# Kernel tuning notes

Measured on AMD Instinct MI355X. Metric: run time of the kernel, lower is better.

## Reference

```python
import jax, jax.numpy as jnp
import numpy as np

# Static graph-batch geometry (equal-size graphs -> uniform per-graph k, jit-friendly)
B = 512        # number of graphs
N_PER = 2048   # nodes per graph
C = 64         # in_channels
DEG = 16       # average degree
K = 1024       # ceil(ratio * N_PER) with ratio = 0.5
N = B * N_PER
E = B * N_PER * DEG


def setup_inputs() -> dict:
    key = jax.random.key(0)
    k1, k2, k3 = jax.random.split(key, 3)
    x = jax.random.normal(k1, (N, C), dtype=jnp.float32)
    # edges are intra-graph: local endpoints in [0, N_PER) plus per-graph node offset
    local = jax.random.randint(k2, (2, E), 0, N_PER, dtype=jnp.int32)
    offs = jnp.repeat(jnp.arange(B, dtype=jnp.int32) * N_PER, N_PER * DEG)
    edge_index = local + offs[None, :]
    batch = jnp.repeat(jnp.arange(B, dtype=jnp.int32), N_PER)
    p = jax.random.normal(k3, (C,), dtype=jnp.float32)  # SelectTopK projection weight
    return {"x": x, "edge_index": edge_index, "batch": batch, "p": p}


def reference(x, edge_index, batch, p):
    # SelectTopK: y = tanh(x @ p / ||p||), per-graph top-k
    y = jnp.tanh(x @ p / jnp.linalg.norm(p))            # [N]
    scores, local_idx = jax.lax.top_k(y.reshape(B, N_PER), K)   # [B, K] each
    perm = (local_idx.astype(jnp.int32)
            + jnp.arange(B, dtype=jnp.int32)[:, None] * N_PER).reshape(-1)  # [B*K] global ids
    score = scores.reshape(-1)                          # [B*K]
    # gather + scale (multiplier == 1)
    x_out = x[perm] * score[:, None]                    # [B*K, C]
    # FilterEdges / connect: remap kept nodes to new contiguous ids, mask dropped edges
    node_map = jnp.full((N,), -1, dtype=jnp.int32).at[perm].set(
        jnp.arange(B * K, dtype=jnp.int32))
    new_src = node_map[edge_index[0]]
    new_dst = node_map[edge_index[1]]
    edge_mask = (new_src >= 0) & (new_dst >= 0)         # [E] which edges survive
    new_edge_index = jnp.where(edge_mask[None, :],
                               jnp.stack([new_src, new_dst]), -1)  # dropped edges = -1
    new_batch = batch[perm]
    return x_out, new_edge_index, new_batch, perm, score
```

## Files before the change

### kernel.cpp

```cpp
#include <hip/hip_runtime.h>
#include <cstdint>
#include <cstddef>

#define NB 512
#define N_PER 2048
#define NC 64
#define DEG 16
#define KSEL 1024
#define NTOT (NB * N_PER)
#define ETOT (NTOT * DEG)
#define NOUT (NB * KSEL)

#define T 512
#define EPT 4


__global__ __launch_bounds__(T) void fused_topk_kernel(
    const float* __restrict__ x, const float* __restrict__ p,
    const int* __restrict__ ei,
    float* __restrict__ out_x, float* __restrict__ out_edge,
    float* __restrict__ out_batch, float* __restrict__ out_perm,
    float* __restrict__ out_score) {
  __shared__ unsigned long long key2[EPT][T];
  __shared__ int lmap[N_PER];
  __shared__ int klist[KSEL];
  __shared__ float kscore[KSEL];
  __shared__ double p_s[NC];
  __shared__ double norm_s;

  const int tid = threadIdx.x;
  const int b = blockIdx.x;
  const int base = b * N_PER;

  if (tid < NC) p_s[tid] = (double)p[tid];
  __syncthreads();
  if (tid == 0) {
    double s = 0.0;
    for (int i = 0; i < NC; ++i) s += p_s[i] * p_s[i];
    norm_s = sqrt(s);
  }

  const int lane = tid & 15;
  const int rowg = tid >> 4;
  const double pw0 = p_s[lane * 4 + 0];
  const double pw1 = p_s[lane * 4 + 1];
  const double pw2 = p_s[lane * 4 + 2];
  const double pw3 = p_s[lane * 4 + 3];
  const float4* xrow = (const float4*)(x + (size_t)base * NC);

  for (int r0 = 0; r0 < N_PER; r0 += 32) {
    const int row = r0 + rowg;
    float4 v = xrow[row * 16 + lane];
    double part = (double)v.x * pw0 + (double)v.y * pw1 +
                  (double)v.z * pw2 + (double)v.w * pw3;
    part += __shfl_xor(part, 8, 16);
    part += __shfl_xor(part, 4, 16);
    part += __shfl_xor(part, 2, 16);
    part += __shfl_xor(part, 1, 16);
    if (lane == 0) {
      unsigned long long u = (unsigned long long)__double_as_longlong(part);
      unsigned long long asc =
          (u & 0x8000000000000000ULL) ? ~u : (u | 0x8000000000000000ULL);
      unsigned long long desc = ~asc;
      key2[row & 3][row >> 2] = (desc & ~2047ULL) | (unsigned long long)row;
    }
  }
  __syncthreads();

  unsigned long long r[EPT];
#pragma unroll
  for (int s = 0; s < EPT; ++s) r[s] = key2[s][tid];

  auto CE = [](unsigned long long& a, unsigned long long& c, bool up) {
    if ((a > c) == up) { unsigned long long t = a; a = c; c = t; }
  };
  auto shfl_stage = [&](int m, bool up) {
    const bool keepmin = (((tid & m) == 0) == up);
#pragma unroll
    for (int s = 0; s < EPT; ++s) {
      unsigned long long o = __shfl_xor(r[s], m, 64);
      const bool take = keepmin ? (o < r[s]) : (o > r[s]);
      if (take) r[s] = o;
    }
  };
  auto lds_stage = [&](int m, bool up) {
    __syncthreads();
#pragma unroll
    for (int s = 0; s < EPT; ++s) key2[s][tid] = r[s];
    __syncthreads();
    const bool keepmin = (((tid & m) == 0) == up);
#pragma unroll
    for (int s = 0; s < EPT; ++s) {
      unsigned long long o = key2[s][tid ^ m];
      const bool take = keepmin ? (o < r[s]) : (o > r[s]);
      if (take) r[s] = o;
    }
  };

  CE(r[0], r[1], true);
  CE(r[2], r[3], false);
  {
    const bool up = ((tid & 1) == 0);
    CE(r[0], r[2], up); CE(r[1], r[3], up);
    CE(r[0], r[1], up); CE(r[2], r[3], up);
  }
#pragma unroll
  for (int k = 8; k <= N_PER; k <<= 1) {
    const bool up = ((tid & (k >> 2)) == 0);
#pragma unroll
    for (int j = (k >> 1); j >= 256; j >>= 1) lds_stage(j >> 2, up);
#pragma unroll
    for (int j = ((k >> 1) > 128 ? 128 : (k >> 1)); j >= 4; j >>= 1)
      shfl_stage(j >> 2, up);
    CE(r[0], r[2], up); CE(r[1], r[3], up);
    CE(r[0], r[1], up); CE(r[2], r[3], up);
  }

  __syncthreads();
  const double norm = norm_s;
#pragma unroll
  for (int s = 0; s < EPT; ++s) {
    const int pos = tid * EPT + s;
    const int idx = (int)(r[s] & 2047ULL);
    if (pos < KSEL) {
      unsigned long long desc = r[s] & ~2047ULL;
      unsigned long long asc = ~desc;
      unsigned long long u = (asc & 0x8000000000000000ULL)
                                 ? (asc ^ 0x8000000000000000ULL)
                                 : ~asc;
      const double dot = __longlong_as_double((long long)u);
      const float sc = tanhf((float)(dot / norm));
      const int nid = b * KSEL + pos;
      out_batch[nid] = (float)b;
      out_perm[nid] = (float)(base + idx);
      out_score[nid] = sc;
      klist[pos] = idx;
      kscore[pos] = sc;
      lmap[idx] = nid;
    } else {
      lmap[idx] = -1;
    }
  }
  __syncthreads();

  const float4* xg = (const float4*)x;
  float4* xo = (float4*)out_x;
#pragma unroll 4
  for (int rr = 0; rr < KSEL; rr += 32) {
    const int row = rr + rowg;
    const int idx = klist[row];
    const float sc = kscore[row];
    float4 v = xg[(size_t)(base + idx) * 16 + lane];
    v.x *= sc; v.y *= sc; v.z *= sc; v.w *= sc;
    xo[(size_t)(b * KSEL + row) * 16 + lane] = v;
  }

  const int nE4 = N_PER * DEG / 4;
  const int4* s_ei = (const int4*)ei + (size_t)b * nE4;
  const int4* d_ei = (const int4*)(ei + (size_t)ETOT) + (size_t)b * nE4;
  float4* o_s = (float4*)out_edge + (size_t)b * nE4;
  float4* o_d = (float4*)(out_edge + (size_t)ETOT) + (size_t)b * nE4;
#pragma unroll 2
  for (int i = tid; i < nE4; i += T) {
    const int4 s4 = s_ei[i];
    const int4 d4 = d_ei[i];
    const int ns0 = lmap[s4.x - base], ns1 = lmap[s4.y - base];
    const int ns2 = lmap[s4.z - base], ns3 = lmap[s4.w - base];
    const int nd0 = lmap[d4.x - base], nd1 = lmap[d4.y - base];
    const int nd2 = lmap[d4.z - base], nd3 = lmap[d4.w - base];
    float4 os, od;
    const bool k0 = (ns0 >= 0) && (nd0 >= 0);
    const bool k1 = (ns1 >= 0) && (nd1 >= 0);
    const bool k2 = (ns2 >= 0) && (nd2 >= 0);
    const bool k3 = (ns3 >= 0) && (nd3 >= 0);
    os.x = k0 ? (float)ns0 : -1.0f; od.x = k0 ? (float)nd0 : -1.0f;
    os.y = k1 ? (float)ns1 : -1.0f; od.y = k1 ? (float)nd1 : -1.0f;
    os.z = k2 ? (float)ns2 : -1.0f; od.z = k2 ? (float)nd2 : -1.0f;
    os.w = k3 ? (float)ns3 : -1.0f; od.w = k3 ? (float)nd3 : -1.0f;
    o_s[i] = os;
    o_d[i] = od;
  }
}

extern "C" void kernel_launch(void* const* d_in, const int* in_sizes, int n_in,
                              void* d_out, int out_size, void* d_ws,
                              size_t ws_size, hipStream_t stream) {
  const float* x = (const float*)d_in[0];
  const int* ei = (const int*)d_in[1];
  const float* p = (const float*)d_in[3];

  float* out = (float*)d_out;
  float* out_x = out;
  float* out_edge = out + 33554432;
  float* out_batch = out + 67108864;
  float* out_perm = out + 67633152;
  float* out_score = out + 68157440;

  fused_topk_kernel<<<NB, T, 0, stream>>>(x, p, ei, out_x, out_edge, out_batch,
                                          out_perm, out_score);
}
```

Baseline: 572.4 us.

## Double block size to 1024 threads with two keys per thread in bitonic sort

Raises the block to 1024 threads and halves the per-thread sort register array from four to two keys, remapping the in-register, shuffle and shared-memory bitonic stages to match. Row-strided loops for the projection and gather advance by 64 rows instead of 32. The aim is more threads in flight per block for latency hiding in the memory-bound phases and lower register pressure. The cost is more LDS exchange stages and more block-wide barriers in the sort.

```diff
diff --git a/kernel.cpp b/kernel.cpp
--- a/kernel.cpp
+++ b/kernel.cpp
@@ -11,11 +11,11 @@
 #define ETOT (NTOT * DEG)
 #define NOUT (NB * KSEL)
 
-#define T 512
-#define EPT 4
+#define T 1024
+#define EPT 2
 
 
-__global__ __launch_bounds__(T) void fused_topk_kernel(
+__global__ __launch_bounds__(T, 8) void fused_topk_kernel(
     const float* __restrict__ x, const float* __restrict__ p,
     const int* __restrict__ ei,
     float* __restrict__ out_x, float* __restrict__ out_edge,
@@ -48,7 +48,7 @@
   const double pw3 = p_s[lane * 4 + 3];
   const float4* xrow = (const float4*)(x + (size_t)base * NC);
 
-  for (int r0 = 0; r0 < N_PER; r0 += 32) {
+  for (int r0 = 0; r0 < N_PER; r0 += 64) {
     const int row = r0 + rowg;
     float4 v = xrow[row * 16 + lane];
     double part = (double)v.x * pw0 + (double)v.y * pw1 +
@@ -62,68 +62,57 @@
       unsigned long long asc =
           (u & 0x8000000000000000ULL) ? ~u : (u | 0x8000000000000000ULL);
       unsigned long long desc = ~asc;
-      key2[row & 3][row >> 2] = (desc & ~2047ULL) | (unsigned long long)row;
+      key2[row & 1][row >> 1] = (desc & ~2047ULL) | (unsigned long long)row;
     }
   }
   __syncthreads();
 
-  unsigned long long r[EPT];
-#pragma unroll
-  for (int s = 0; s < EPT; ++s) r[s] = key2[s][tid];
+  unsigned long long r0k = key2[0][tid];
+  unsigned long long r1k = key2[1][tid];
 
   auto CE = [](unsigned long long& a, unsigned long long& c, bool up) {
     if ((a > c) == up) { unsigned long long t = a; a = c; c = t; }
   };
   auto shfl_stage = [&](int m, bool up) {
     const bool keepmin = (((tid & m) == 0) == up);
-#pragma unroll
-    for (int s = 0; s < EPT; ++s) {
-      unsigned long long o = __shfl_xor(r[s], m, 64);
-      const bool take = keepmin ? (o < r[s]) : (o > r[s]);
-      if (take) r[s] = o;
-    }
+    unsigned long long o0 = __shfl_xor(r0k, m, 64);
+    unsigned long long o1 = __shfl_xor(r1k, m, 64);
+    if (keepmin ? (o0 < r0k) : (o0 > r0k)) r0k = o0;
+    if (keepmin ? (o1 < r1k) : (o1 > r1k)) r1k = o1;
   };
   auto lds_stage = [&](int m, bool up) {
     __syncthreads();
-#pragma unroll
-    for (int s = 0; s < EPT; ++s) key2[s][tid] = r[s];
+    key2[0][tid] = r0k;
+    key2[1][tid] = r1k;
     __syncthreads();
     const bool keepmin = (((tid & m) == 0) == up);
-#pragma unroll
-    for (int s = 0; s < EPT; ++s) {
-      unsigned long long o = key2[s][tid ^ m];
-      const bool take = keepmin ? (o < r[s]) : (o > r[s]);
-      if (take) r[s] = o;
-    }
+    unsigned long long o0 = key2[0][tid ^ m];
+    unsigned long long o1 = key2[1][tid ^ m];
+    if (keepmin ? (o0 < r0k) : (o0 > r0k)) r0k = o0;
+    if (keepmin ? (o1 < r1k) : (o1 > r1k)) r1k = o1;
   };
 
-  CE(r[0], r[1], true);
-  CE(r[2], r[3], false);
-  {
-    const bool up = ((tid & 1) == 0);
-    CE(r[0], r[2], up); CE(r[1], r[3], up);
-    CE(r[0], r[1], up); CE(r[2], r[3], up);
-  }
+  CE(r0k, r1k, (tid & 1) == 0);
 #pragma unroll
-  for (int k = 8; k <= N_PER; k <<= 1) {
-    const bool up = ((tid & (k >> 2)) == 0);
+  for (int k = 4; k <= N_PER; k <<= 1) {
+    const bool up = ((tid & (k >> 1)) == 0);
 #pragma unroll
-    for (int j = (k >> 1); j >= 256; j >>= 1) lds_stage(j >> 2, up);
+    for (int j = (k >> 1); j >= 128; j >>= 1) lds_stage(j >> 1, up);
 #pragma unroll
-    for (int j = ((k >> 1) > 128 ? 128 : (k >> 1)); j >= 4; j >>= 1)
-      shfl_stage(j >> 2, up);
-    CE(r[0], r[2], up); CE(r[1], r[3], up);
-    CE(r[0], r[1], up); CE(r[2], r[3], up);
+    for (int j = ((k >> 1) > 64 ? 64 : (k >> 1)); j >= 2; j >>= 1)
+      shfl_stage(j >> 1, up);
+    CE(r0k, r1k, up);
   }
 
   __syncthreads();
   const double norm = norm_s;
 #pragma unroll
   for (int s = 0; s < EPT; ++s) {
+    const unsigned long long key = (s == 0) ? r0k : r1k;
     const int pos = tid * EPT + s;
-    const int idx = (int)(r[s] & 2047ULL);
+    const int idx = (int)(key & 2047ULL);
     if (pos < KSEL) {
-      unsigned long long desc = r[s] & ~2047ULL;
+      unsigned long long desc = key & ~2047ULL;
       unsigned long long asc = ~desc;
       unsigned long long u = (asc & 0x8000000000000000ULL)
                                  ? (asc ^ 0x8000000000000000ULL)
@@ -146,7 +135,7 @@
   const float4* xg = (const float4*)x;
   float4* xo = (float4*)out_x;
 #pragma unroll 4
-  for (int rr = 0; rr < KSEL; rr += 32) {
+  for (int rr = 0; rr < KSEL; rr += 64) {
     const int row = rr + rowg;
     const int idx = klist[row];
     const float sc = kscore[row];
```

After: 576.7 us. Within noise of the previous version (+0.7%).
